# Kernel tuning notes

Measured on AMD Instinct MI355X. Metric: run time of the kernel, lower is better.

## Reference

```python
import jax, jax.numpy as jnp
import numpy as np

B, NPG, IN_DIM, HID, H, DEG, NTYPE, NLAYERS = 4, 5000, 16, 128, 8, 32, 12, 4
N = B * NPG
DH = HID // H
E = N * DEG + N  # random edges + self loops


def setup_inputs() -> dict:
    key = jax.random.key(0)
    ks = jax.random.split(key, 10)
    e_rand = N * DEG
    # intra-graph random edges: sample within [0, NPG) then offset by graph id
    src = jax.random.randint(ks[0], (e_rand,), 0, NPG, dtype=jnp.int32)
    dst = jax.random.randint(ks[1], (e_rand,), 0, NPG, dtype=jnp.int32)
    gid = jnp.repeat(jnp.arange(B, dtype=jnp.int32), NPG * DEG) * NPG
    loops = jnp.arange(N, dtype=jnp.int32)
    edge_index = jnp.stack([jnp.concatenate([src + gid, loops]),
                            jnp.concatenate([dst + gid, loops])])
    edge_type = jnp.concatenate([
        jax.random.randint(ks[2], (e_rand,), 1, NTYPE, dtype=jnp.int32),
        jnp.zeros((N,), jnp.int32)])  # self-loop type = 0
    feat = jax.random.normal(ks[3], (N, IN_DIM), jnp.float32)
    s = 0.1
    return {
        "feat": feat,
        "edge_table": jax.random.normal(ks[4], (NTYPE, HID), jnp.float32) * s,
        "W_embed": jax.random.normal(ks[5], (IN_DIM, HID), jnp.float32) * s,
        "b_embed": jnp.zeros((HID,), jnp.float32),
        "W_conv": jax.random.normal(ks[6], (HID, HID), jnp.float32) * s,
        "a_src": jax.random.normal(ks[7], (H, DH), jnp.float32) * s,
        "a_dst": jax.random.normal(ks[8], (H, DH), jnp.float32) * s,
        "a_edge": jax.random.normal(ks[9], (H, DH), jnp.float32) * s,
        "edge_index": edge_index,
        "edge_type": edge_type,
    }


def _forward(feat, edge_table, W_embed, b_embed, W_conv, a_src, a_dst, a_edge,
             edge_index, edge_type):
    src, dst = edge_index[0], edge_index[1]
    # feature masking done in the torch forward
    feat = feat.at[:, 2:4].set(0.0).at[:, 10:].set(0.0)
    # 'sum'-flavor edge embedding: type lookup -> [E, H, DH]
    e_feat = edge_table[edge_type].reshape(-1, H, DH)
    ea = jnp.sum(e_feat * a_edge, axis=-1)  # [E, H]
    h = jax.nn.gelu(feat @ W_embed + b_embed)  # node embedder MLP
    layers = [feat, h]
    for _ in range(NLAYERS):  # shared_conv=True: same weights each layer
        z = (h @ W_conv).reshape(N, H, DH)
        s_logit = jnp.sum(z * a_src, axis=-1)  # [N, H]
        d_logit = jnp.sum(z * a_dst, axis=-1)
        logit = jax.nn.leaky_relu(s_logit[src] + d_logit[dst] + ea, 0.2)
        # numerically-stable edge softmax over incoming edges of each dst
        m = jax.ops.segment_max(logit, dst, num_segments=N)
        ex = jnp.exp(logit - jax.lax.stop_gradient(m)[dst])
        denom = jax.ops.segment_sum(ex, dst, num_segments=N)
        alpha = ex / (denom[dst] + 1e-9)  # [E, H]
        msg = alpha[..., None] * z[src]  # [E, H, DH]
        agg = jax.ops.segment_sum(msg, dst, num_segments=N).reshape(N, HID)
        h = h + jax.nn.gelu(agg)  # residual
        layers.append(h)
    feats_all = jnp.concatenate(layers, axis=1)  # layer_pooling='all' -> [N, 656]
    nf = feats_all.reshape(B, NPG, -1)
    g_emb = jnp.max(nf, axis=1, keepdims=True)  # graph_pooling='max'
    return jnp.concatenate([nf, jnp.broadcast_to(g_emb, nf.shape)], axis=2)


def reference(feat, edge_table, W_embed, b_embed, W_conv, a_src, a_dst, a_edge,
              edge_index, edge_type):
    return _forward(feat, edge_table, W_embed, b_embed, W_conv, a_src, a_dst,
                    a_edge, edge_index, edge_type)
```

## Files before the change

### kernel.cpp

```cpp
#include <hip/hip_runtime.h>
#include <math.h>

#define IN_DIM 16
#define HIDN 128
#define NH 8
#define DHD 16
#define NTYPE 12
#define NLAYERS 4
#define NPG 5000
#define NSEGP 250
#define RPS (NPG / NSEGP)
#define C1 656
#define C2 1312
#define C1Q (C1 / 4)
#define CAP 64
#define NPW 4
#define HREG (NPG / 2)
#define GEMM_SLOTS ((HREG + 63) / 64)
#define EDGE_SLOTS (HREG / NPW)

typedef float vf4 __attribute__((ext_vector_type(4)));

__device__ __forceinline__ float gelu_t(float x) {
    float x3 = x * x * x;
    float u = 0.7978845608028654f * (x + 0.044715f * x3);
    return 0.5f * x * (1.0f + tanhf(u));
}

__device__ __forceinline__ unsigned pack_bf16(float lo, float hi) {
    unsigned a = __float_as_uint(lo);
    unsigned b = __float_as_uint(hi);
    a = (a + 0x7fffu + ((a >> 16) & 1u)) >> 16;
    b = (b + 0x7fffu + ((b >> 16) & 1u)) & 0xffff0000u;
    return a | b;
}

__device__ __forceinline__ float lrelu(float x) { return (x >= 0.f) ? x : 0.2f * x; }

__global__ __launch_bounds__(256) void k_init(const float* __restrict__ etab,
                                              const float* __restrict__ aed,
                                              float* __restrict__ ea, int* __restrict__ cnt,
                                              int N) {
    int i = blockIdx.x * 256 + threadIdx.x;
    if (i < NTYPE * NH) {
        int t = i / NH, hh = i % NH;
        float s = 0.f;
        #pragma unroll
        for (int d = 0; d < DHD; d++) s += etab[t * HIDN + hh * DHD + d] * aed[hh * DHD + d];
        ea[i] = s;
    }
    if (i < N) cnt[i] = 0;
}

__global__ __launch_bounds__(256) void k_pre(const float* __restrict__ feat,
                                             const float* __restrict__ We,
                                             const float* __restrict__ be,
                                             const int* __restrict__ srcp,
                                             const int* __restrict__ dstp,
                                             const int* __restrict__ etp,
                                             int* __restrict__ cnt,
                                             unsigned* __restrict__ payload2,
                                             float* __restrict__ out, int N, int E) {
    int bid = blockIdx.x, tid = threadIdx.x;
    int wave = tid >> 6, lane = tid & 63;
    int n = bid * NPW + wave;
    if (n < N) {
        float v = 0.f;
        if (lane < IN_DIM) {
            v = feat[n * IN_DIM + lane];
            if ((lane >= 2 && lane < 4) || lane >= 10) v = 0.f;
            out[(size_t)n * C2 + lane] = v;
        }
        float a0 = be[lane], a1 = be[lane + 64];
        #pragma unroll
        for (int k = 0; k < IN_DIM; k++) {
            float fk = __shfl(v, k);
            a0 += fk * We[k * HIDN + lane];
            a1 += fk * We[k * HIDN + lane + 64];
        }
        size_t ob = (size_t)n * C2 + IN_DIM;
        out[ob + lane] = gelu_t(a0);
        out[ob + lane + 64] = gelu_t(a1);
    }
    for (int e = bid * 256 + tid; e < E; e += gridDim.x * 256) {
        int d = dstp[e];
        int slot = atomicAdd(&cnt[d], 1);
        if (slot < CAP) {
            unsigned pk = (unsigned)srcp[e] | ((unsigned)etp[e] << 16);
            __builtin_nontemporal_store(pk, &payload2[(size_t)d * CAP + slot]);
        }
    }
}

#define KC 64
__global__ __launch_bounds__(256) void k_gemm(const float* __restrict__ out,
                                              const float* __restrict__ W,
                                              const float* __restrict__ asf,
                                              const float* __restrict__ adf,
                                              unsigned* __restrict__ z16,
                                              float* __restrict__ slog,
                                              float* __restrict__ dlog, int prevbase, int N) {
    __shared__ float WcA[KC][64];
    __shared__ float WcB[KC][64];
    __shared__ float hc[64][KC + 4];
    int xcd = blockIdx.x & 7, slot = blockIdx.x >> 3;
    int g = xcd & 3, half = xcd >> 2;
    int base = g * NPG + half * HREG;
    int rend = base + HREG;
    int n0 = base + slot * 64;
    int t = threadIdx.x;
    int cg = t & 15, rg = t >> 4;
    int c0 = cg * 8;
    const float* hin = out + prevbase;
    float acc[4][8];
    #pragma unroll
    for (int i = 0; i < 4; i++)
        #pragma unroll
        for (int j = 0; j < 8; j++) acc[i][j] = 0.f;

    for (int k0 = 0; k0 < HIDN; k0 += KC) {
        for (int i = t; i < KC * 32; i += 256) {
            int kk = i >> 5, cc = (i & 31) << 2;
            float4 v = *(const float4*)&W[(k0 + kk) * HIDN + cc];
            int halfcol = (cc & ~4) >> 1;
            if (cc & 4) *(float4*)&WcB[kk][halfcol] = v;
            else *(float4*)&WcA[kk][halfcol] = v;
        }
        for (int i = t; i < 64 * (KC / 4); i += 256) {
            int rr = i / (KC / 4), kk = (i % (KC / 4)) * 4;
            int n = n0 + rr;
            float4 v = make_float4(0.f, 0.f, 0.f, 0.f);
            if (n < rend) v = *(const float4*)&hin[(size_t)n * C2 + k0 + kk];
            *(float4*)&hc[rr][kk] = v;
        }
        __syncthreads();
        for (int k = 0; k < KC; k++) {
            float4 w0 = *(float4*)&WcA[k][cg * 4];
            float4 w1 = *(float4*)&WcB[k][cg * 4];
            float hv[4];
            #pragma unroll
            for (int i = 0; i < 4; i++) hv[i] = hc[rg + 16 * i][k];
            #pragma unroll
            for (int i = 0; i < 4; i++) {
                acc[i][0] += hv[i] * w0.x;
                acc[i][1] += hv[i] * w0.y;
                acc[i][2] += hv[i] * w0.z;
                acc[i][3] += hv[i] * w0.w;
                acc[i][4] += hv[i] * w1.x;
                acc[i][5] += hv[i] * w1.y;
                acc[i][6] += hv[i] * w1.z;
                acc[i][7] += hv[i] * w1.w;
            }
        }
        __syncthreads();
    }
    float4 s0 = *(const float4*)&asf[c0];
    float4 s1 = *(const float4*)&asf[c0 + 4];
    float4 d0 = *(const float4*)&adf[c0];
    float4 d1 = *(const float4*)&adf[c0 + 4];
    #pragma unroll
    for (int i = 0; i < 4; i++) {
        int n = n0 + rg + 16 * i;
        float ps = acc[i][0] * s0.x + acc[i][1] * s0.y + acc[i][2] * s0.z + acc[i][3] * s0.w +
                   acc[i][4] * s1.x + acc[i][5] * s1.y + acc[i][6] * s1.z + acc[i][7] * s1.w;
        float pd = acc[i][0] * d0.x + acc[i][1] * d0.y + acc[i][2] * d0.z + acc[i][3] * d0.w +
                   acc[i][4] * d1.x + acc[i][5] * d1.y + acc[i][6] * d1.z + acc[i][7] * d1.w;
        ps += __shfl_xor(ps, 1);
        pd += __shfl_xor(pd, 1);
        unsigned u[8];
        #pragma unroll
        for (int j = 0; j < 8; j++) {
            float other = __shfl_xor(acc[i][j], 8);
            u[j] = pack_bf16(acc[i][j], other);
        }
        if (n < rend) {
            if (cg < 8) {
                *(uint4*)&z16[(size_t)n * 64 + c0] = make_uint4(u[0], u[1], u[2], u[3]);
                *(uint4*)&z16[(size_t)n * 64 + c0 + 4] = make_uint4(u[4], u[5], u[6], u[7]);
            }
            if ((cg & 1) == 0) {
                slog[n * NH + (cg >> 1)] = ps;
                dlog[n * NH + (cg >> 1)] = pd;
            }
        }
    }
}

__global__ __launch_bounds__(256) void k_edge(const int* __restrict__ cnt,
                                              const unsigned* __restrict__ payload2,
                                              const float* __restrict__ slog,
                                              const float* __restrict__ dlog,
                                              const float* __restrict__ ea,
                                              const unsigned* __restrict__ z16,
                                              float* __restrict__ out, int prevbase,
                                              int curbase, int N) {
    int wave = threadIdx.x >> 6, lane = threadIdx.x & 63;
    int xcd = blockIdx.x & 7, slot = blockIdx.x >> 3;
    int g = xcd & 3, half = xcd >> 2;
    int unit = g * (NPG / NPW) + half * EDGE_SLOTS + slot;
    int n = unit * NPW + wave;
    bool active = (n < N);
    __shared__ float lbuf[NPW][CAP * NH];
    __shared__ unsigned pbuf[NPW][CAP];
    __shared__ float dl[NPW][NH];
    __shared__ float red[NPW][NH];
    __shared__ float sea[NTYPE * NH];

    if (threadIdx.x < NTYPE * NH) sea[threadIdx.x] = ea[threadIdx.x];

    int cntE = 0;
    if (active) {
        cntE = cnt[n];
        if (cntE > CAP) cntE = CAP;
        if (lane < NH) dl[wave][lane] = dlog[n * NH + lane];
    }
    if (lane < cntE) pbuf[wave][lane] = payload2[(size_t)n * CAP + lane];
    __syncthreads();

    int o = lane & 1;
    int eoff = lane >> 1;
    float4 dl4 = *(float4*)&dl[wave][o * 4];
    float4 ssum4 = make_float4(0.f, 0.f, 0.f, 0.f);
    #pragma unroll
    for (int base = 0; base < CAP; base += 32) {
        int el = base + eoff;
        if (el < cntE) {
            unsigned pk = pbuf[wave][el];
            int src = pk & 0xffff;
            int et = pk >> 16;
            float4 s4 = *(const float4*)&slog[src * NH + o * 4];
            float4 e4 = *(float4*)&sea[et * NH + o * 4];
            float4 ex;
            ex.x = __expf(lrelu(s4.x + dl4.x + e4.x));
            ex.y = __expf(lrelu(s4.y + dl4.y + e4.y));
            ex.z = __expf(lrelu(s4.z + dl4.z + e4.z));
            ex.w = __expf(lrelu(s4.w + dl4.w + e4.w));
            *(float4*)&lbuf[wave][el * NH + o * 4] = ex;
            ssum4.x += ex.x;
            ssum4.y += ex.y;
            ssum4.z += ex.z;
            ssum4.w += ex.w;
        }
    }
    #pragma unroll
    for (int m = 2; m <= 32; m <<= 1) {
        ssum4.x += __shfl_xor(ssum4.x, m);
        ssum4.y += __shfl_xor(ssum4.y, m);
        ssum4.z += __shfl_xor(ssum4.z, m);
        ssum4.w += __shfl_xor(ssum4.w, m);
    }
    if (lane < 2) {
        float4 r4;
        r4.x = 1.0f / (ssum4.x + 1e-9f);
        r4.y = 1.0f / (ssum4.y + 1e-9f);
        r4.z = 1.0f / (ssum4.z + 1e-9f);
        r4.w = 1.0f / (ssum4.w + 1e-9f);
        *(float4*)&red[wave][o * 4] = r4;
    }
    __syncthreads();

    int h1 = lane >> 4, h2 = h1 + 4;
    float r1 = red[wave][h1], r2 = red[wave][h2];
    float a0 = 0.f, a1 = 0.f;
    int e = 0;
    for (; e + 7 < cntE; e += 8) {
        unsigned v[8];
        #pragma unroll
        for (int j = 0; j < 8; j++) {
            unsigned s = pbuf[wave][e + j] & 0xffff;
            v[j] = z16[(size_t)s * 64 + lane];
        }
        #pragma unroll
        for (int j = 0; j < 8; j++) {
            float l0 = lbuf[wave][(e + j) * NH + h1];
            float l1 = lbuf[wave][(e + j) * NH + h2];
            a0 += l0 * __uint_as_float(v[j] << 16);
            a1 += l1 * __uint_as_float(v[j] & 0xffff0000u);
        }
    }
    for (; e < cntE; e++) {
        unsigned s0 = pbuf[wave][e] & 0xffff;
        unsigned v0 = z16[(size_t)s0 * 64 + lane];
        a0 += lbuf[wave][e * NH + h1] * __uint_as_float(v0 << 16);
        a1 += lbuf[wave][e * NH + h2] * __uint_as_float(v0 & 0xffff0000u);
    }
    if (active) {
        a0 *= r1;
        a1 *= r2;
        size_t rowb = (size_t)n * C2;
        float o0 = out[rowb + prevbase + lane] + gelu_t(a0);
        float o1 = out[rowb + prevbase + lane + 64] + gelu_t(a1);
        out[rowb + curbase + lane] = o0;
        out[rowb + curbase + lane + 64] = o1;
    }
}

__global__ __launch_bounds__(256) void k_pool_partial(const float* __restrict__ out,
                                                      float* __restrict__ gpart) {
    int xcd = blockIdx.x & 7, slot = blockIdx.x >> 3;
    int b = xcd & 3, half = xcd >> 2;
    int seg = half * (NSEGP / 2) + slot;
    int n0 = b * NPG + seg * RPS;
    for (int c = threadIdx.x; c < C1; c += 256) {
        float m = -3.4e38f;
        #pragma unroll
        for (int i = 0; i < RPS; i++) m = fmaxf(m, out[(size_t)(n0 + i) * C2 + c]);
        gpart[(size_t)(b * NSEGP + seg) * C1 + c] = m;
    }
}

__global__ __launch_bounds__(256) void k_pool_final(const float* __restrict__ gpart,
                                                    float* __restrict__ gemb, int B) {
    int w = blockIdx.x * 4 + (threadIdx.x >> 6);
    int lane = threadIdx.x & 63;
    if (w >= B * C1) return;
    int b = w / C1, c = w % C1;
    float m = -3.4e38f;
    for (int s = lane; s < NSEGP; s += 64) m = fmaxf(m, gpart[(size_t)(b * NSEGP + s) * C1 + c]);
    #pragma unroll
    for (int k = 1; k < 64; k <<= 1) m = fmaxf(m, __shfl_xor(m, k));
    if (lane == 0) gemb[w] = m;
}

__global__ __launch_bounds__(256) void k_bcast(const float* __restrict__ gemb,
                                               float* __restrict__ out, int N) {
    int idx = blockIdx.x * 256 + threadIdx.x;
    if (idx < N * C1Q) {
        int n = idx / C1Q, c4 = idx % C1Q;
        int b = n / NPG;
        vf4 g = *(const vf4*)&gemb[b * C1 + c4 * 4];
        __builtin_nontemporal_store(g, (vf4*)&out[(size_t)n * C2 + C1 + c4 * 4]);
    }
}

extern "C" void kernel_launch(void* const* d_in, const int* in_sizes, int n_in, void* d_out,
                              int out_size, void* d_ws, size_t ws_size, hipStream_t stream) {
    const float* feat = (const float*)d_in[0];
    const float* etab = (const float*)d_in[1];
    const float* We = (const float*)d_in[2];
    const float* be = (const float*)d_in[3];
    const float* Wc = (const float*)d_in[4];
    const float* a_src = (const float*)d_in[5];
    const float* a_dst = (const float*)d_in[6];
    const float* a_edge = (const float*)d_in[7];
    const int* eidx = (const int*)d_in[8];
    const int* etype = (const int*)d_in[9];
    float* out = (float*)d_out;

    const int N = in_sizes[0] / IN_DIM;
    const int E = in_sizes[9];
    const int B = N / NPG;

    const int* srcp = eidx;
    const int* dstp = eidx + E;

    char* w = (char*)d_ws;
    size_t off = 0;
    auto carve = [&](size_t bytes) {
        char* p = w + off;
        off = (off + bytes + 255) & ~(size_t)255;
        return p;
    };
    unsigned* z16 = (unsigned*)carve((size_t)N * 64 * 4);
    float* slog = (float*)carve((size_t)N * NH * 4);
    float* dlog = (float*)carve((size_t)N * NH * 4);
    float* ea = (float*)carve(NTYPE * NH * 4);
    int* cnt = (int*)carve((size_t)N * 4);
    unsigned* payload2 = (unsigned*)carve((size_t)N * CAP * 4);
    float* gpart = (float*)carve((size_t)B * NSEGP * C1 * 4);
    float* gemb = (float*)carve((size_t)B * C1 * 4);
    (void)ws_size;

    k_init<<<(N + 255) / 256, 256, 0, stream>>>(etab, a_edge, ea, cnt, N);
    k_pre<<<(N + NPW - 1) / NPW, 256, 0, stream>>>(feat, We, be, srcp, dstp, etype, cnt,
                                                   payload2, out, N, E);

    for (int l = 0; l < NLAYERS; l++) {
        int prevbase = IN_DIM + HIDN * l;
        int curbase = IN_DIM + HIDN * (l + 1);
        k_gemm<<<8 * GEMM_SLOTS, 256, 0, stream>>>(out, Wc, a_src, a_dst, z16, slog, dlog,
                                                   prevbase, N);
        k_edge<<<8 * EDGE_SLOTS, 256, 0, stream>>>(cnt, payload2, slog, dlog, ea, z16, out,
                                                   prevbase, curbase, N);
    }

    k_pool_partial<<<8 * (NSEGP / 2), 256, 0, stream>>>(out, gpart);
    k_pool_final<<<(B * C1 + 3) / 4, 256, 0, stream>>>(gpart, gemb, B);
    k_bcast<<<((size_t)N * C1Q + 255) / 256, 256, 0, stream>>>(gemb, out, N);
}
```

Measured before the change: 257.4 us.

## Fuse graph max-pool partials into last edge layer and grid-stride broadcast

The separate partial max-pool kernel is removed. The last edge-aggregation launch now writes per-4-node partial maxima: columns of the newest layer come from registers via shared memory, and older columns are reread from the output rows it just touched. The final reduction now scans 1250 partials per graph instead of 250, and the broadcast kernel uses a fixed 2048-block grid-stride loop. This saves one launch and one full pass over the output, but it adds a block-wide barrier and extra global reads to the edge kernel, and it makes the final reduction larger.

```diff
diff --git a/kernel.cpp b/kernel.cpp
--- a/kernel.cpp
+++ b/kernel.cpp
@@ -8,8 +8,6 @@
 #define NTYPE 12
 #define NLAYERS 4
 #define NPG 5000
-#define NSEGP 250
-#define RPS (NPG / NSEGP)
 #define C1 656
 #define C2 1312
 #define C1Q (C1 / 4)
@@ -18,6 +16,8 @@
 #define HREG (NPG / 2)
 #define GEMM_SLOTS ((HREG + 63) / 64)
 #define EDGE_SLOTS (HREG / NPW)
+#define NSEG2 (NPG / NPW)
+#define POOLBASE 528
 
 typedef float vf4 __attribute__((ext_vector_type(4)));
 
@@ -192,9 +192,11 @@
                                               const float* __restrict__ dlog,
                                               const float* __restrict__ ea,
                                               const unsigned* __restrict__ z16,
-                                              float* __restrict__ out, int prevbase,
-                                              int curbase, int N) {
-    int wave = threadIdx.x >> 6, lane = threadIdx.x & 63;
+                                              float* __restrict__ out,
+                                              float* __restrict__ gpart, int prevbase,
+                                              int curbase, int dopool, int N) {
+    int tid = threadIdx.x;
+    int wave = tid >> 6, lane = tid & 63;
     int xcd = blockIdx.x & 7, slot = blockIdx.x >> 3;
     int g = xcd & 3, half = xcd >> 2;
     int unit = g * (NPG / NPW) + half * EDGE_SLOTS + slot;
@@ -205,8 +207,9 @@
     __shared__ float dl[NPW][NH];
     __shared__ float red[NPW][NH];
     __shared__ float sea[NTYPE * NH];
-
-    if (threadIdx.x < NTYPE * NH) sea[threadIdx.x] = ea[threadIdx.x];
+    __shared__ float pm[NPW][HIDN];
+
+    if (tid < NTYPE * NH) sea[tid] = ea[tid];
 
     int cntE = 0;
     if (active) {
@@ -284,28 +287,35 @@
         a0 += lbuf[wave][e * NH + h1] * __uint_as_float(v0 << 16);
         a1 += lbuf[wave][e * NH + h2] * __uint_as_float(v0 & 0xffff0000u);
     }
+    float o0 = 0.f, o1 = 0.f;
     if (active) {
         a0 *= r1;
         a1 *= r2;
         size_t rowb = (size_t)n * C2;
-        float o0 = out[rowb + prevbase + lane] + gelu_t(a0);
-        float o1 = out[rowb + prevbase + lane + 64] + gelu_t(a1);
+        o0 = out[rowb + prevbase + lane] + gelu_t(a0);
+        o1 = out[rowb + prevbase + lane + 64] + gelu_t(a1);
         out[rowb + curbase + lane] = o0;
         out[rowb + curbase + lane + 64] = o1;
     }
-}
-
-__global__ __launch_bounds__(256) void k_pool_partial(const float* __restrict__ out,
-                                                      float* __restrict__ gpart) {
-    int xcd = blockIdx.x & 7, slot = blockIdx.x >> 3;
-    int b = xcd & 3, half = xcd >> 2;
-    int seg = half * (NSEGP / 2) + slot;
-    int n0 = b * NPG + seg * RPS;
-    for (int c = threadIdx.x; c < C1; c += 256) {
-        float m = -3.4e38f;
-        #pragma unroll
-        for (int i = 0; i < RPS; i++) m = fmaxf(m, out[(size_t)(n0 + i) * C2 + c]);
-        gpart[(size_t)(b * NSEGP + seg) * C1 + c] = m;
+    if (dopool) {
+        pm[wave][lane] = active ? o0 : -3.4e38f;
+        pm[wave][lane + 64] = active ? o1 : -3.4e38f;
+        __syncthreads();
+        for (int c = tid; c < C1; c += 256) {
+            float m;
+            if (c < POOLBASE) {
+                m = -3.4e38f;
+                #pragma unroll
+                for (int r = 0; r < NPW; r++) {
+                    int nn = unit * NPW + r;
+                    if (nn < N) m = fmaxf(m, out[(size_t)nn * C2 + c]);
+                }
+            } else {
+                int cc = c - POOLBASE;
+                m = fmaxf(fmaxf(pm[0][cc], pm[1][cc]), fmaxf(pm[2][cc], pm[3][cc]));
+            }
+            gpart[(size_t)unit * C1 + c] = m;
+        }
     }
 }
 
@@ -316,7 +326,7 @@
     if (w >= B * C1) return;
     int b = w / C1, c = w % C1;
     float m = -3.4e38f;
-    for (int s = lane; s < NSEGP; s += 64) m = fmaxf(m, gpart[(size_t)(b * NSEGP + s) * C1 + c]);
+    for (int s = lane; s < NSEG2; s += 64) m = fmaxf(m, gpart[(size_t)(b * NSEG2 + s) * C1 + c]);
     #pragma unroll
     for (int k = 1; k < 64; k <<= 1) m = fmaxf(m, __shfl_xor(m, k));
     if (lane == 0) gemb[w] = m;
@@ -324,8 +334,9 @@
 
 __global__ __launch_bounds__(256) void k_bcast(const float* __restrict__ gemb,
                                                float* __restrict__ out, int N) {
-    int idx = blockIdx.x * 256 + threadIdx.x;
-    if (idx < N * C1Q) {
+    size_t total = (size_t)N * C1Q;
+    for (size_t idx = (size_t)blockIdx.x * 256 + threadIdx.x; idx < total;
+         idx += (size_t)gridDim.x * 256) {
         int n = idx / C1Q, c4 = idx % C1Q;
         int b = n / NPG;
         vf4 g = *(const vf4*)&gemb[b * C1 + c4 * 4];
@@ -367,7 +378,7 @@
     float* ea = (float*)carve(NTYPE * NH * 4);
     int* cnt = (int*)carve((size_t)N * 4);
     unsigned* payload2 = (unsigned*)carve((size_t)N * CAP * 4);
-    float* gpart = (float*)carve((size_t)B * NSEGP * C1 * 4);
+    float* gpart = (float*)carve((size_t)B * NSEG2 * C1 * 4);
     float* gemb = (float*)carve((size_t)B * C1 * 4);
     (void)ws_size;
 
@@ -381,10 +392,10 @@
         k_gemm<<<8 * GEMM_SLOTS, 256, 0, stream>>>(out, Wc, a_src, a_dst, z16, slog, dlog,
                                                    prevbase, N);
         k_edge<<<8 * EDGE_SLOTS, 256, 0, stream>>>(cnt, payload2, slog, dlog, ea, z16, out,
-                                                   prevbase, curbase, N);
-    }
-
-    k_pool_partial<<<8 * (NSEGP / 2), 256, 0, stream>>>(out, gpart);
+                                                   gpart, prevbase, curbase,
+                                                   (l == NLAYERS - 1) ? 1 : 0, N);
+    }
+
     k_pool_final<<<(B * C1 + 3) / 4, 256, 0, stream>>>(gpart, gemb, B);
-    k_bcast<<<((size_t)N * C1Q + 255) / 256, 256, 0, stream>>>(gemb, out, N);
-}
+    k_bcast<<<2048, 256, 0, stream>>>(gemb, out, N);
+}
```

New measurement: 271.2 us. 1.05x slower.
